# Kernel tuning notes

Measured on AMD Instinct MI355X. Metric: run time of the kernel, lower is better.

Reference implementation:

```python
import jax, jax.numpy as jnp
import numpy as np

VOCAB = 50257
EMBED = 512
HIDDEN = 1024
UNITS = HIDDEN // 2  # per-direction LSTM units
B, S, T = 32, 8, 128


def _lstm_bias(units):
    # Keras unit_forget_bias=True: bias = [0 (i), 1 (f), 0 (c), 0 (o)]
    return jnp.concatenate([jnp.zeros((units,)), jnp.ones((units,)),
                            jnp.zeros((2 * units,))])


def setup_inputs() -> dict:
    key = jax.random.key(0)
    ks = jax.random.split(key, 8)
    # token ids with variable-length zero padding (pad_token_id=0)
    x = jax.random.randint(ks[0], (B, S, T), 1, VOCAB)
    lengths = jax.random.randint(ks[1], (B, S, 1), T // 2, T + 1)
    pos = jnp.arange(T)[None, None, :]
    x = jnp.where(pos < lengths, x, 0).astype(jnp.int32)

    emb_table = jax.random.normal(ks[2], (VOCAB, EMBED), jnp.float32) * 0.05

    def glorot(k, shape):
        fan = np.sqrt(2.0 / (shape[0] + shape[1]))
        return jax.random.normal(k, shape, jnp.float32) * fan

    W_f = glorot(ks[3], (EMBED, 4 * UNITS))
    U_f = glorot(ks[4], (UNITS, 4 * UNITS))
    W_b = glorot(ks[5], (EMBED, 4 * UNITS))
    U_b = glorot(ks[6], (UNITS, 4 * UNITS))
    b_f = _lstm_bias(UNITS)
    b_b = _lstm_bias(UNITS)
    return {"x": x, "emb_table": emb_table,
            "W_f": W_f, "U_f": U_f, "b_f": b_f,
            "W_b": W_b, "U_b": U_b, "b_b": b_b}


def _masked_lstm_final(xW, mask, U):
    """xW: (N, T, 4u) precomputed input projections (+bias); mask: (N, T) bool.
    Returns final hidden state (N, u) with Keras masking semantics: masked
    timesteps are skipped (state held)."""
    N = xW.shape[0]
    u = U.shape[0]
    h0 = jnp.zeros((N, u), xW.dtype)
    c0 = jnp.zeros((N, u), xW.dtype)

    def step(carry, inp):
        h, c = carry
        z, m = inp  # z: (N, 4u), m: (N,)
        z = z + h @ U
        i, f, g, o = jnp.split(z, 4, axis=-1)
        i = jax.nn.sigmoid(i)
        f = jax.nn.sigmoid(f)
        g = jnp.tanh(g)
        o = jax.nn.sigmoid(o)
        c_new = f * c + i * g
        h_new = o * jnp.tanh(c_new)
        m = m[:, None]
        return (jnp.where(m, h_new, h), jnp.where(m, c_new, c)), None

    (hT, _), _ = jax.lax.scan(
        step, (h0, c0),
        (jnp.swapaxes(xW, 0, 1), jnp.swapaxes(mask, 0, 1)))
    return hT


def reference(x, emb_table, W_f, U_f, b_f, W_b, U_b, b_b):
    Bx, Sx, Tx = x.shape
    N = Bx * Sx
    ids = x.reshape(N, Tx)
    mask = ids != 0  # mask_zero=True
    emb = emb_table[ids]  # (N, T, E)

    # forward direction
    xWf = emb @ W_f + b_f  # (N, T, 4u), one big GEMM up front
    h_fwd = _masked_lstm_final(xWf, mask, U_f)

    # backward direction: reverse time and mask (Keras go_backwards)
    emb_rev = emb[:, ::-1, :]
    mask_rev = mask[:, ::-1]
    xWb = emb_rev @ W_b + b_b
    h_bwd = _masked_lstm_final(xWb, mask_rev, U_b)

    out = jnp.concatenate([h_fwd, h_bwd], axis=-1)  # (N, hidden_dim)
    return out.reshape(Bx, Sx, HIDDEN)
```

## Files before the change

### kernel.cpp

```cpp
#include <hip/hip_runtime.h>

typedef _Float16 half_t;
typedef _Float16 half8 __attribute__((ext_vector_type(8)));
typedef float floatx4 __attribute__((ext_vector_type(4)));

#define NSEQ   256
#define TLEN   128
#define EMBD   512
#define UNITSZ 512
#define GC     2048
#define NTOK   32768
#define NCOL   4096
#define KDIM   512

constexpr size_t OFF_EMB = 0;
constexpr size_t OFF_WT  = 33554432;
constexpr size_t OFF_UT  = OFF_WT + 4194304;
constexpr size_t OFF_HB  = OFF_UT + 4194304;
constexpr size_t OFF_CNT = OFF_HB + 1048576;
constexpr size_t OFF_MSK = OFF_CNT + 4096;
constexpr size_t OFF_XW  = OFF_MSK + 4096;

__device__ inline float sigm(float x)  { return 1.0f / (1.0f + __expf(-x)); }
__device__ inline float tanhx(float x) { return 2.0f / (1.0f + __expf(-2.0f * x)) - 1.0f; }

__device__ inline unsigned long long ld8c(const void* p) {
    return __hip_atomic_load((const unsigned long long*)p, __ATOMIC_RELAXED, __HIP_MEMORY_SCOPE_AGENT);
}
__device__ inline void st8c(void* p, unsigned long long v) {
    __hip_atomic_store((unsigned long long*)p, v, __ATOMIC_RELAXED, __HIP_MEMORY_SCOPE_AGENT);
}

__global__ void pack_kernel(const float* __restrict__ Wf, const float* __restrict__ Uf,
                            const float* __restrict__ Wb, const float* __restrict__ Ub,
                            half_t* __restrict__ WT, half_t* __restrict__ UT) {
    int c = blockIdx.x * 256 + threadIdx.x;
    int arr = c >> 18;
    int r = c & 262143;
    int kc = r >> 12;
    int gc = r & 4095;
    int dir = gc >> 11;
    int g = gc & 2047;
    const float* src = (arr == 0) ? (dir ? Wb : Wf) : (dir ? Ub : Uf);
    half_t* dst = (arr == 0) ? WT : UT;
    half8 v;
#pragma unroll
    for (int j = 0; j < 8; ++j)
        v[j] = (half_t)src[(size_t)(kc * 8 + j) * GC + g];
    *(half8*)(dst + (size_t)gc * KDIM + kc * 8) = v;
}

__global__ void zero_kernel(unsigned* __restrict__ hb_and_cnt) {
    int i = blockIdx.x * 256 + threadIdx.x;
    if (i < 263168) hb_and_cnt[i] = 0u;
}

__global__ void mask_kernel(const int* __restrict__ x, unsigned long long* __restrict__ mk) {
    int n = blockIdx.x;
    int l = threadIdx.x;
    unsigned long long b0 = __ballot(x[n * TLEN + l] != 0);
    unsigned long long b1 = __ballot(x[n * TLEN + 64 + l] != 0);
    if (l == 0) { mk[n * 2] = b0; mk[n * 2 + 1] = b1; }
}

__global__ void gather_kernel(const int* __restrict__ x, const float* __restrict__ tab,
                              half_t* __restrict__ embf) {
    int g = blockIdx.x * 256 + threadIdx.x;
    int token = g >> 6;
    int k = (g & 63) * 8;
    int id = x[token];
    const float* s = tab + (size_t)id * EMBD + k;
    float4 a = *(const float4*)(s);
    float4 b = *(const float4*)(s + 4);
    half8 v;
    v[0] = (half_t)a.x; v[1] = (half_t)a.y; v[2] = (half_t)a.z; v[3] = (half_t)a.w;
    v[4] = (half_t)b.x; v[5] = (half_t)b.y; v[6] = (half_t)b.z; v[7] = (half_t)b.w;
    *(half8*)(embf + (size_t)token * EMBD + k) = v;
}

__global__ __launch_bounds__(256, 2) void gemm_kernel(const half_t* __restrict__ embf,
                                                      const half_t* __restrict__ WT,
                                                      const float* __restrict__ bf,
                                                      const float* __restrict__ bb,
                                                      half_t* __restrict__ xw) {
    __shared__ half_t As[128 * 40];
    __shared__ half_t Bs[128 * 40];
    int bx = blockIdx.x;
    int bm = bx & 255, bn = bx >> 8;
    int r0 = bm * 128, c0 = bn * 128;
    int tid = threadIdx.x;
    int w = tid >> 6, l = tid & 63;
    int q = l >> 4, cl = l & 15;
    int mq = (w >> 1) * 64, nq = (w & 1) * 64;

    floatx4 acc[4][4];
#pragma unroll
    for (int a = 0; a < 4; ++a)
#pragma unroll
        for (int b = 0; b < 4; ++b) acc[a][b] = (floatx4){0.f, 0.f, 0.f, 0.f};

    for (int kb = 0; kb < 16; ++kb) {
#pragma unroll
        for (int cc = 0; cc < 2; ++cc) {
            int c = tid + cc * 256;
            int row = c >> 2, qt = c & 3;
            half8 va = *(const half8*)(embf + (size_t)(r0 + row) * KDIM + kb * 32 + qt * 8);
            *(half8*)(As + row * 40 + qt * 8) = va;
            half8 vb = *(const half8*)(WT + (size_t)(c0 + row) * KDIM + kb * 32 + qt * 8);
            *(half8*)(Bs + row * 40 + qt * 8) = vb;
        }
        __syncthreads();
        half8 af[4], bfr[4];
#pragma unroll
        for (int mb = 0; mb < 4; ++mb)
            af[mb] = *(const half8*)(As + (mq + mb * 16 + cl) * 40 + q * 8);
#pragma unroll
        for (int nb = 0; nb < 4; ++nb)
            bfr[nb] = *(const half8*)(Bs + (nq + nb * 16 + cl) * 40 + q * 8);
#pragma unroll
        for (int mb = 0; mb < 4; ++mb)
#pragma unroll
            for (int nb = 0; nb < 4; ++nb)
                acc[mb][nb] = __builtin_amdgcn_mfma_f32_16x16x32_f16(af[mb], bfr[nb], acc[mb][nb], 0, 0, 0);
        __syncthreads();
    }
#pragma unroll
    for (int nb = 0; nb < 4; ++nb) {
        int col = c0 + nq + nb * 16 + cl;
        int dir = col >> 11, gcol = col & 2047;
        float bias = dir ? bb[gcol] : bf[gcol];
#pragma unroll
        for (int mb = 0; mb < 4; ++mb) {
#pragma unroll
            for (int r = 0; r < 4; ++r) {
                int row = r0 + mq + mb * 16 + q * 4 + r;
                xw[(size_t)row * NCOL + col] = (half_t)(acc[mb][nb][r] + bias);
            }
        }
    }
}

__global__ __launch_bounds__(256, 1) void lstm_kernel(const half_t* __restrict__ xw,
                                                      const half_t* __restrict__ UT,
                                                      half_t* __restrict__ hbuf,
                                                      const unsigned long long* __restrict__ mk,
                                                      float* __restrict__ out,
                                                      unsigned* __restrict__ cnt) {
    __shared__ half_t Ast[8192];
    __shared__ half_t Pk[1024];
    int bx = blockIdx.x;
    int dir = bx >> 7;
    int rowg = (bx >> 3) & 15;
    int wgc = bx & 7;
    int tid = threadIdx.x;
    int w = tid >> 6, l = tid & 63;
    int q = l >> 4, cl = l & 15;
    int cg = wgc * 4 + w;
    int ub = cg * 16;
    int ub0 = wgc * 64;
    int r0 = rowg * 16;

    half8 bfrag[64];
#pragma unroll
    for (int kk = 0; kk < 16; ++kk)
#pragma unroll
        for (int cf = 0; cf < 4; ++cf)
            bfrag[kk * 4 + cf] = *(const half8*)(UT + (size_t)(dir * 2048 + cf * 512 + ub + cl) * KDIM + kk * 32 + q * 8);

    unsigned long long mlo[4], mhi[4];
#pragma unroll
    for (int r = 0; r < 4; ++r) {
        int n = r0 + q * 4 + r;
        mlo[r] = mk[n * 2];
        mhi[r] = mk[n * 2 + 1];
    }

    float cs[4] = {0.f, 0.f, 0.f, 0.f};
    float hs[4] = {0.f, 0.f, 0.f, 0.f};
    unsigned* cptr = cnt + (dir * 16 + rowg) * 16;
    int colb = dir * 2048 + ub + cl;

    half_t xv[4][4];
    {
        int tIdx = dir ? 127 : 0;
#pragma unroll
        for (int r = 0; r < 4; ++r) {
            size_t ro = ((size_t)(r0 + q * 4 + r) * TLEN + tIdx) * NCOL;
#pragma unroll
            for (int g = 0; g < 4; ++g)
                xv[g][r] = xw[ro + colb + g * 512];
        }
    }

#pragma unroll 1
    for (int t = 0; t < TLEN; ++t) {
        int tIdx = dir ? (127 - t) : t;
        int rpar = t & 1, wpar = rpar ^ 1;
        if (t > 0) {
            if (tid == 0) {
                while (__hip_atomic_load(cptr, __ATOMIC_RELAXED, __HIP_MEMORY_SCOPE_AGENT) < (unsigned)(32 * t))
                    __builtin_amdgcn_s_sleep(1);
            }
            __syncthreads();
        }
        const half_t* hsrc = hbuf + (size_t)(dir * 2 + rpar) * NSEQ * UNITSZ;
#pragma unroll
        for (int cc = 0; cc < 4; ++cc) {
            int c = tid + cc * 256;
            int kk = c >> 6, ll = c & 63;
            int m = ll & 15, koff = kk * 32 + (ll >> 4) * 8;
            const half_t* sp = hsrc + (size_t)(r0 + m) * UNITSZ + koff;
            union { unsigned long long u[2]; half8 v; } cv;
            cv.u[0] = ld8c(sp);
            cv.u[1] = ld8c(sp + 4);
            *(half8*)(Ast + c * 8) = cv.v;
        }
        __syncthreads();
        floatx4 a0, a1, a2, a3;
#pragma unroll
        for (int r = 0; r < 4; ++r) {
            a0[r] = (float)xv[0][r];
            a1[r] = (float)xv[1][r];
            a2[r] = (float)xv[2][r];
            a3[r] = (float)xv[3][r];
        }
#pragma unroll
        for (int kk = 0; kk < 16; ++kk) {
            half8 af = *(const half8*)(Ast + (kk * 64 + l) * 8);
            a0 = __builtin_amdgcn_mfma_f32_16x16x32_f16(af, bfrag[kk * 4 + 0], a0, 0, 0, 0);
            a1 = __builtin_amdgcn_mfma_f32_16x16x32_f16(af, bfrag[kk * 4 + 1], a1, 0, 0, 0);
            a2 = __builtin_amdgcn_mfma_f32_16x16x32_f16(af, bfrag[kk * 4 + 2], a2, 0, 0, 0);
            a3 = __builtin_amdgcn_mfma_f32_16x16x32_f16(af, bfrag[kk * 4 + 3], a3, 0, 0, 0);
        }
#pragma unroll
        for (int r = 0; r < 4; ++r) {
            unsigned long long mw = (tIdx & 64) ? mhi[r] : mlo[r];
            bool keep = (mw >> (tIdx & 63)) & 1ull;
            float iv = sigm(a0[r]);
            float fv = sigm(a1[r]);
            float gv = tanhx(a2[r]);
            float ov = sigm(a3[r]);
            float cn = fv * cs[r] + iv * gv;
            float hn = ov * tanhx(cn);
            if (keep) { cs[r] = cn; hs[r] = hn; }
            Pk[(q * 4 + r) * 64 + w * 16 + cl] = (half_t)hs[r];
        }
        __syncthreads();
        half_t* hdst = hbuf + (size_t)(dir * 2 + wpar) * NSEQ * UNITSZ;
        {
            int prow = tid >> 4, pch = tid & 15;
            unsigned long long pv = *(const unsigned long long*)(Pk + prow * 64 + pch * 4);
            st8c(hdst + (size_t)(r0 + prow) * UNITSZ + ub0 + pch * 4, pv);
        }
        asm volatile("s_waitcnt vmcnt(0)" ::: "memory");
        if (l == 0)
            __hip_atomic_fetch_add(cptr, 1u, __ATOMIC_RELAXED, __HIP_MEMORY_SCOPE_AGENT);
        if (t + 1 < TLEN) {
            int tN = dir ? (126 - t) : (t + 1);
#pragma unroll
            for (int r = 0; r < 4; ++r) {
                size_t ro = ((size_t)(r0 + q * 4 + r) * TLEN + tN) * NCOL;
#pragma unroll
                for (int g = 0; g < 4; ++g)
                    xv[g][r] = xw[ro + colb + g * 512];
            }
        }
    }
#pragma unroll
    for (int r = 0; r < 4; ++r) {
        int n = r0 + q * 4 + r;
        out[(size_t)n * 1024 + dir * 512 + ub + cl] = hs[r];
    }
}

extern "C" void kernel_launch(void* const* d_in, const int* in_sizes, int n_in,
                              void* d_out, int out_size, void* d_ws, size_t ws_size,
                              hipStream_t stream) {
    const int*   x    = (const int*)d_in[0];
    const float* tab  = (const float*)d_in[1];
    const float* Wf   = (const float*)d_in[2];
    const float* Uf   = (const float*)d_in[3];
    const float* bf   = (const float*)d_in[4];
    const float* Wb   = (const float*)d_in[5];
    const float* Ub   = (const float*)d_in[6];
    const float* bb   = (const float*)d_in[7];
    float* out = (float*)d_out;

    char* ws = (char*)d_ws;
    half_t*   embf = (half_t*)(ws + OFF_EMB);
    half_t*   WT   = (half_t*)(ws + OFF_WT);
    half_t*   UT   = (half_t*)(ws + OFF_UT);
    half_t*   hbuf = (half_t*)(ws + OFF_HB);
    unsigned* cnt  = (unsigned*)(ws + OFF_CNT);
    unsigned long long* mkb = (unsigned long long*)(ws + OFF_MSK);
    half_t*   xw   = (half_t*)(ws + OFF_XW);
    unsigned* hbz  = (unsigned*)(ws + OFF_HB);

    pack_kernel<<<2048, 256, 0, stream>>>(Wf, Uf, Wb, Ub, WT, UT);
    zero_kernel<<<1028, 256, 0, stream>>>(hbz);
    mask_kernel<<<256, 64, 0, stream>>>(x, mkb);
    gather_kernel<<<8192, 256, 0, stream>>>(x, tab, embf);
    gemm_kernel<<<8192, 256, 0, stream>>>(embf, WT, bf, bb, xw);
    lstm_kernel<<<256, 256, 0, stream>>>(xw, UT, hbuf, mkb, out, cnt);
}
```

Before: 1.100 ms.

## Drop LDS staging and block barriers in LSTM recurrence; per-wave spin and direct loads

The recurrent LSTM kernel no longer stages h through shared memory or uses __syncthreads. Each wave now spins on the group counter itself, loads its A fragments straight from global memory with cache-bypassing asm loads, and stores h values directly as shorts. The next step's xW loads are issued before the MFMAs so their latency overlaps compute. Block-to-group mapping is interleaved and counters are padded further apart. The spin loop has an iteration cap, so an unusually long wait would let a wave proceed with stale h. More waves now poll the counter and more small global transactions are issued.

```diff
diff --git a/kernel.cpp b/kernel.cpp
--- a/kernel.cpp
+++ b/kernel.cpp
@@ -24,11 +24,67 @@
 __device__ inline float sigm(float x)  { return 1.0f / (1.0f + __expf(-x)); }
 __device__ inline float tanhx(float x) { return 2.0f / (1.0f + __expf(-2.0f * x)) - 1.0f; }
 
-__device__ inline unsigned long long ld8c(const void* p) {
-    return __hip_atomic_load((const unsigned long long*)p, __ATOMIC_RELAXED, __HIP_MEMORY_SCOPE_AGENT);
-}
-__device__ inline void st8c(void* p, unsigned long long v) {
-    __hip_atomic_store((unsigned long long*)p, v, __ATOMIC_RELAXED, __HIP_MEMORY_SCOPE_AGENT);
+__device__ inline unsigned ld_cnt(const unsigned* p) {
+    unsigned v;
+    asm volatile("global_load_dword %0, %1, off sc0 sc1\n\t"
+                 "s_waitcnt vmcnt(0)" : "=v"(v) : "v"(p) : "memory");
+    return v;
+}
+
+__device__ inline void st_h(unsigned short* p, unsigned v) {
+    asm volatile("global_store_short %0, %1, off sc0 sc1" :: "v"(p), "v"(v) : "memory");
+}
+
+__device__ inline void af_issue(const half_t* ap, half8* af) {
+    asm volatile(
+        "global_load_dwordx4 %0, %16, off sc0 sc1\n\t"
+        "global_load_dwordx4 %1, %16, off offset:64 sc0 sc1\n\t"
+        "global_load_dwordx4 %2, %16, off offset:128 sc0 sc1\n\t"
+        "global_load_dwordx4 %3, %16, off offset:192 sc0 sc1\n\t"
+        "global_load_dwordx4 %4, %16, off offset:256 sc0 sc1\n\t"
+        "global_load_dwordx4 %5, %16, off offset:320 sc0 sc1\n\t"
+        "global_load_dwordx4 %6, %16, off offset:384 sc0 sc1\n\t"
+        "global_load_dwordx4 %7, %16, off offset:448 sc0 sc1\n\t"
+        "global_load_dwordx4 %8, %16, off offset:512 sc0 sc1\n\t"
+        "global_load_dwordx4 %9, %16, off offset:576 sc0 sc1\n\t"
+        "global_load_dwordx4 %10, %16, off offset:640 sc0 sc1\n\t"
+        "global_load_dwordx4 %11, %16, off offset:704 sc0 sc1\n\t"
+        "global_load_dwordx4 %12, %16, off offset:768 sc0 sc1\n\t"
+        "global_load_dwordx4 %13, %16, off offset:832 sc0 sc1\n\t"
+        "global_load_dwordx4 %14, %16, off offset:896 sc0 sc1\n\t"
+        "global_load_dwordx4 %15, %16, off offset:960 sc0 sc1"
+        : "=&v"(af[0]), "=&v"(af[1]), "=&v"(af[2]), "=&v"(af[3]),
+          "=&v"(af[4]), "=&v"(af[5]), "=&v"(af[6]), "=&v"(af[7]),
+          "=&v"(af[8]), "=&v"(af[9]), "=&v"(af[10]), "=&v"(af[11]),
+          "=&v"(af[12]), "=&v"(af[13]), "=&v"(af[14]), "=&v"(af[15])
+        : "v"(ap) : "memory");
+}
+
+__device__ inline void xv_issue(const half_t* p0, const half_t* p1,
+                                const half_t* p2, const half_t* p3,
+                                unsigned* xvr) {
+    asm volatile(
+        "global_load_ushort %0, %16, off\n\t"
+        "global_load_ushort %1, %16, off offset:1024\n\t"
+        "global_load_ushort %2, %16, off offset:2048\n\t"
+        "global_load_ushort %3, %16, off offset:3072\n\t"
+        "global_load_ushort %4, %17, off\n\t"
+        "global_load_ushort %5, %17, off offset:1024\n\t"
+        "global_load_ushort %6, %17, off offset:2048\n\t"
+        "global_load_ushort %7, %17, off offset:3072\n\t"
+        "global_load_ushort %8, %18, off\n\t"
+        "global_load_ushort %9, %18, off offset:1024\n\t"
+        "global_load_ushort %10, %18, off offset:2048\n\t"
+        "global_load_ushort %11, %18, off offset:3072\n\t"
+        "global_load_ushort %12, %19, off\n\t"
+        "global_load_ushort %13, %19, off offset:1024\n\t"
+        "global_load_ushort %14, %19, off offset:2048\n\t"
+        "global_load_ushort %15, %19, off offset:3072"
+        : "=&v"(xvr[0]), "=&v"(xvr[1]), "=&v"(xvr[2]), "=&v"(xvr[3]),
+          "=&v"(xvr[4]), "=&v"(xvr[5]), "=&v"(xvr[6]), "=&v"(xvr[7]),
+          "=&v"(xvr[8]), "=&v"(xvr[9]), "=&v"(xvr[10]), "=&v"(xvr[11]),
+          "=&v"(xvr[12]), "=&v"(xvr[13]), "=&v"(xvr[14]), "=&v"(xvr[15])
+        : "v"(p0), "v"(p1), "v"(p2), "v"(p3) : "memory");
 }
 
 __global__ void pack_kernel(const float* __restrict__ Wf, const float* __restrict__ Uf,
@@ -146,18 +202,16 @@
                                                       const unsigned long long* __restrict__ mk,
                                                       float* __restrict__ out,
                                                       unsigned* __restrict__ cnt) {
-    __shared__ half_t Ast[8192];
-    __shared__ half_t Pk[1024];
     int bx = blockIdx.x;
-    int dir = bx >> 7;
-    int rowg = (bx >> 3) & 15;
-    int wgc = bx & 7;
+    int grp = bx & 31;
+    int wgc = bx >> 5;
+    int dir = grp >> 4;
+    int rowg = grp & 15;
     int tid = threadIdx.x;
     int w = tid >> 6, l = tid & 63;
     int q = l >> 4, cl = l & 15;
     int cg = wgc * 4 + w;
     int ub = cg * 16;
-    int ub0 = wgc * 64;
     int r0 = rowg * 16;
 
     half8 bfrag[64];
@@ -177,61 +231,67 @@
 
     float cs[4] = {0.f, 0.f, 0.f, 0.f};
     float hs[4] = {0.f, 0.f, 0.f, 0.f};
-    unsigned* cptr = cnt + (dir * 16 + rowg) * 16;
+    unsigned* cptr = cnt + grp * 32;
     int colb = dir * 2048 + ub + cl;
 
-    half_t xv[4][4];
+    const half_t* ap0 = hbuf + (size_t)(dir * 2 + 0) * NSEQ * UNITSZ + (size_t)(r0 + cl) * UNITSZ + q * 8;
+    const half_t* ap1 = ap0 + (size_t)NSEQ * UNITSZ;
+    half_t* hw0 = hbuf + (size_t)(dir * 2 + 0) * NSEQ * UNITSZ + (size_t)(r0 + q * 4) * UNITSZ + ub + cl;
+    half_t* hw1 = hw0 + (size_t)NSEQ * UNITSZ;
+
+    const half_t* xb0 = xw + (size_t)(r0 + q * 4 + 0) * TLEN * NCOL + colb;
+    const half_t* xb1 = xw + (size_t)(r0 + q * 4 + 1) * TLEN * NCOL + colb;
+    const half_t* xb2 = xw + (size_t)(r0 + q * 4 + 2) * TLEN * NCOL + colb;
+    const half_t* xb3 = xw + (size_t)(r0 + q * 4 + 3) * TLEN * NCOL + colb;
+
+    unsigned xvr[16];
     {
-        int tIdx = dir ? 127 : 0;
-#pragma unroll
-        for (int r = 0; r < 4; ++r) {
-            size_t ro = ((size_t)(r0 + q * 4 + r) * TLEN + tIdx) * NCOL;
-#pragma unroll
-            for (int g = 0; g < 4; ++g)
-                xv[g][r] = xw[ro + colb + g * 512];
-        }
-    }
+        int tI = dir ? 127 : 0;
+        xv_issue(xb0 + (size_t)tI * NCOL, xb1 + (size_t)tI * NCOL,
+                 xb2 + (size_t)tI * NCOL, xb3 + (size_t)tI * NCOL, xvr);
+    }
+    asm volatile("s_waitcnt vmcnt(0)" ::: "memory");
+    __builtin_amdgcn_sched_barrier(0);
 
 #pragma unroll 1
     for (int t = 0; t < TLEN; ++t) {
         int tIdx = dir ? (127 - t) : t;
-        int rpar = t & 1, wpar = rpar ^ 1;
+        int rpar = t & 1;
+        floatx4 a0, a1, a2, a3;
+#pragma unroll
+        for (int r = 0; r < 4; ++r) {
+            a0[r] = (float)__builtin_bit_cast(half_t, (unsigned short)xvr[r * 4 + 0]);
+            a1[r] = (float)__builtin_bit_cast(half_t, (unsigned short)xvr[r * 4 + 1]);
+            a2[r] = (float)__builtin_bit_cast(half_t, (unsigned short)xvr[r * 4 + 2]);
+            a3[r] = (float)__builtin_bit_cast(half_t, (unsigned short)xvr[r * 4 + 3]);
+        }
+        half8 af[16];
         if (t > 0) {
-            if (tid == 0) {
-                while (__hip_atomic_load(cptr, __ATOMIC_RELAXED, __HIP_MEMORY_SCOPE_AGENT) < (unsigned)(32 * t))
-                    __builtin_amdgcn_s_sleep(1);
+            unsigned tgt = 32u * (unsigned)t;
+            for (unsigned sp = 0;; ++sp) {
+                if (ld_cnt(cptr) >= tgt) break;
+                if (sp >= (1u << 20)) break;
+                __builtin_amdgcn_s_sleep(1);
             }
-            __syncthreads();
-        }
-        const half_t* hsrc = hbuf + (size_t)(dir * 2 + rpar) * NSEQ * UNITSZ;
-#pragma unroll
-        for (int cc = 0; cc < 4; ++cc) {
-            int c = tid + cc * 256;
-            int kk = c >> 6, ll = c & 63;
-            int m = ll & 15, koff = kk * 32 + (ll >> 4) * 8;
-            const half_t* sp = hsrc + (size_t)(r0 + m) * UNITSZ + koff;
-            union { unsigned long long u[2]; half8 v; } cv;
-            cv.u[0] = ld8c(sp);
-            cv.u[1] = ld8c(sp + 4);
-            *(half8*)(Ast + c * 8) = cv.v;
-        }
-        __syncthreads();
-        floatx4 a0, a1, a2, a3;
-#pragma unroll
-        for (int r = 0; r < 4; ++r) {
-            a0[r] = (float)xv[0][r];
-            a1[r] = (float)xv[1][r];
-            a2[r] = (float)xv[2][r];
-            a3[r] = (float)xv[3][r];
-        }
-#pragma unroll
-        for (int kk = 0; kk < 16; ++kk) {
-            half8 af = *(const half8*)(Ast + (kk * 64 + l) * 8);
-            a0 = __builtin_amdgcn_mfma_f32_16x16x32_f16(af, bfrag[kk * 4 + 0], a0, 0, 0, 0);
-            a1 = __builtin_amdgcn_mfma_f32_16x16x32_f16(af, bfrag[kk * 4 + 1], a1, 0, 0, 0);
-            a2 = __builtin_amdgcn_mfma_f32_16x16x32_f16(af, bfrag[kk * 4 + 2], a2, 0, 0, 0);
-            a3 = __builtin_amdgcn_mfma_f32_16x16x32_f16(af, bfrag[kk * 4 + 3], a3, 0, 0, 0);
-        }
+            af_issue(rpar ? ap1 : ap0, af);
+        }
+        {
+            int tN = dir ? (t >= 126 ? 0 : 126 - t) : (t >= 127 ? 127 : t + 1);
+            xv_issue(xb0 + (size_t)tN * NCOL, xb1 + (size_t)tN * NCOL,
+                     xb2 + (size_t)tN * NCOL, xb3 + (size_t)tN * NCOL, xvr);
+        }
+        if (t > 0) {
+            asm volatile("s_waitcnt vmcnt(16)" ::: "memory");
+            __builtin_amdgcn_sched_barrier(0);
+#pragma unroll
+            for (int kk = 0; kk < 16; ++kk) {
+                a0 = __builtin_amdgcn_mfma_f32_16x16x32_f16(af[kk], bfrag[kk * 4 + 0], a0, 0, 0, 0);
+                a1 = __builtin_amdgcn_mfma_f32_16x16x32_f16(af[kk], bfrag[kk * 4 + 1], a1, 0, 0, 0);
+                a2 = __builtin_amdgcn_mfma_f32_16x16x32_f16(af[kk], bfrag[kk * 4 + 2], a2, 0, 0, 0);
+                a3 = __builtin_amdgcn_mfma_f32_16x16x32_f16(af[kk], bfrag[kk * 4 + 3], a3, 0, 0, 0);
+            }
+        }
+        unsigned short* hdst = (unsigned short*)(rpar ? hw0 : hw1);
 #pragma unroll
         for (int r = 0; r < 4; ++r) {
             unsigned long long mw = (tIdx & 64) ? mhi[r] : mlo[r];
@@ -243,28 +303,13 @@
             float cn = fv * cs[r] + iv * gv;
             float hn = ov * tanhx(cn);
             if (keep) { cs[r] = cn; hs[r] = hn; }
-            Pk[(q * 4 + r) * 64 + w * 16 + cl] = (half_t)hs[r];
-        }
-        __syncthreads();
-        half_t* hdst = hbuf + (size_t)(dir * 2 + wpar) * NSEQ * UNITSZ;
-        {
-            int prow = tid >> 4, pch = tid & 15;
-            unsigned long long pv = *(const unsigned long long*)(Pk + prow * 64 + pch * 4);
-            st8c(hdst + (size_t)(r0 + prow) * UNITSZ + ub0 + pch * 4, pv);
+            unsigned hv = (unsigned)__builtin_bit_cast(unsigned short, (half_t)hs[r]);
+            st_h(hdst + r * 512, hv);
         }
         asm volatile("s_waitcnt vmcnt(0)" ::: "memory");
+        __builtin_amdgcn_sched_barrier(0);
         if (l == 0)
             __hip_atomic_fetch_add(cptr, 1u, __ATOMIC_RELAXED, __HIP_MEMORY_SCOPE_AGENT);
-        if (t + 1 < TLEN) {
-            int tN = dir ? (126 - t) : (t + 1);
-#pragma unroll
-            for (int r = 0; r < 4; ++r) {
-                size_t ro = ((size_t)(r0 + q * 4 + r) * TLEN + tN) * NCOL;
-#pragma unroll
-                for (int g = 0; g < 4; ++g)
-                    xv[g][r] = xw[ro + colb + g * 512];
-            }
-        }
     }
 #pragma unroll
     for (int r = 0; r < 4; ++r) {
```

Result: no change. 1.113 ms (+1.2%).
